# Performance work log

Hardware: AMD Instinct MI355X
Metric: run time of the kernel (lower is better)

The kernel has to match this reference:

```python
import jax, jax.numpy as jnp
import numpy as np
import math

B, S, D, H = 2, 2048, 1024, 16
HD = D // H  # head_dim = 64

def setup_inputs() -> dict:
    key = jax.random.key(0)
    ks = jax.random.split(key, 11)
    def n(k, shape, scale=1.0):
        return jax.random.normal(k, shape, dtype=jnp.float32) * scale
    w_scale = 1.0 / math.sqrt(D)
    return {
        "q": n(ks[0], (B, S, D)),
        "k": n(ks[1], (B, S, D)),
        "v": n(ks[2], (B, S, D)),
        "WQ_w": n(ks[3], (D, D), w_scale),
        "WQ_b": n(ks[4], (D,), 0.01),
        "WK_w": n(ks[5], (D, D), w_scale),
        "WK_b": n(ks[6], (D,), 0.01),
        "WV_w": n(ks[7], (D, D), w_scale),
        "WV_b": n(ks[8], (D,), 0.01),
        "Wout_w": n(ks[9], (D, D), w_scale),
        "Wout_b": n(ks[10], (D,), 0.01),
    }

def reference(q, k, v, WQ_w, WQ_b, WK_w, WK_b, WV_w, WV_b, Wout_w, Wout_b):
    b, s, _ = k.shape
    # QKV projections (torch Linear: x @ W.T + b; here weights stored [in, out])
    qh = (q @ WQ_w + WQ_b).reshape(b, -1, H, HD).transpose(0, 2, 1, 3)  # [b,h,s,hd]
    kh = (k @ WK_w + WK_b).reshape(b, -1, H, HD).transpose(0, 2, 1, 3)
    vh = (v @ WV_w + WV_b).reshape(b, -1, H, HD).transpose(0, 2, 1, 3)
    # naive attention: full [b,h,s,s] score matrix
    scores = jnp.einsum("bhqd,bhkd->bhqk", qh, kh) / math.sqrt(HD)
    attn = jax.nn.softmax(scores, axis=-1)
    out = jnp.einsum("bhqk,bhkd->bhqd", attn, vh)
    concat = out.transpose(0, 2, 1, 3).reshape(b, -1, H * HD)  # [b,s,inner_dim]
    return concat @ Wout_w + Wout_b
```

## Files before the change

kernel.cpp:

```cpp
#include <hip/hip_runtime.h>
#include <hip/hip_bf16.h>
#include <stdint.h>

typedef __attribute__((ext_vector_type(8))) short bf16x8;
typedef __attribute__((ext_vector_type(4))) short short4v;
typedef __attribute__((ext_vector_type(4))) float f32x4;

#define MFMA16x16x32 __builtin_amdgcn_mfma_f32_16x16x32_bf16
#define CL2F 0.18033688011112042f

__device__ __forceinline__ short f2b(float f) {
  union { float f; uint32_t u; } x;
  x.f = f;
  uint32_t u = x.u;
  uint32_t r = (u + 0x7FFFu + ((u >> 16) & 1u)) >> 16;
  return (short)(uint16_t)r;
}

__device__ __forceinline__ uint32_t cvt_pk_bf16(float lo, float hi) {
  uint32_t r;
  asm volatile("v_cvt_pk_bf16_f32 %0, %1, %2" : "=v"(r) : "v"(lo), "v"(hi));
  return r;
}
__device__ __forceinline__ float exp2_fast(float x) {
  float r;
  asm volatile("v_exp_f32 %0, %1" : "=v"(r) : "v"(x));
  return r;
}
__device__ __forceinline__ bf16x8 cvt8(const float4 a, const float4 b) {
  union { uint32_t u[4]; bf16x8 v; } o;
  o.u[0] = cvt_pk_bf16(a.x, a.y);
  o.u[1] = cvt_pk_bf16(a.z, a.w);
  o.u[2] = cvt_pk_bf16(b.x, b.y);
  o.u[3] = cvt_pk_bf16(b.z, b.w);
  return o.v;
}

__device__ __forceinline__ void async_copy16(const void* g, void* l) {
  __builtin_amdgcn_global_load_lds(
      (const __attribute__((address_space(1))) void*)g,
      (__attribute__((address_space(3))) void*)l, 16, 0, 0);
}

__global__ void prep_kernel(const float* __restrict__ W0,
                            const float* __restrict__ W1,
                            const float* __restrict__ W2,
                            const float* __restrict__ W3,
                            const float* __restrict__ q,
                            const float* __restrict__ k,
                            const float* __restrict__ v,
                            short* __restrict__ Wt,
                            short* __restrict__ xq,
                            short* __restrict__ xk,
                            short* __restrict__ xv) {
  __shared__ short tile[64][72];
  const int z = blockIdx.z;
  const int t = threadIdx.x;
  if (z < 4) {
    const float* W = (z == 0) ? W0 : (z == 1) ? W1 : (z == 2) ? W2 : W3;
    short* Wo = Wt + (size_t)z * 1024 * 1024;
    const int r0 = blockIdx.y * 64;
    const int c0 = blockIdx.x * 64;
#pragma unroll
    for (int i = 0; i < 4; ++i) {
      const int lin = i * 1024 + t * 4;
      const int r = lin >> 6, c = lin & 63;
      const float4 vv = *(const float4*)&W[(size_t)(r0 + r) * 1024 + c0 + c];
      tile[r][c + 0] = f2b(vv.x);
      tile[r][c + 1] = f2b(vv.y);
      tile[r][c + 2] = f2b(vv.z);
      tile[r][c + 3] = f2b(vv.w);
    }
    __syncthreads();
#pragma unroll
    for (int i = 0; i < 2; ++i) {
      const int lin = i * 2048 + t * 8;
      const int r = lin >> 6, c = lin & 63;
      bf16x8 ov;
#pragma unroll
      for (int jj = 0; jj < 8; ++jj) ov[jj] = tile[c + jj][r];
      *(bf16x8*)&Wo[(size_t)(c0 + r) * 1024 + r0 + c] = ov;
    }
  } else {
    const float* x = (z == 4) ? q : (z == 5) ? k : v;
    short* yp = (z == 4) ? xq : (z == 5) ? xk : xv;
    const int base = (blockIdx.y * 16 + blockIdx.x) * 256 + t;
#pragma unroll
    for (int j = 0; j < 8; ++j) {
      const int i = base + j * 65536;
      const float4 a = ((const float4*)x)[2 * i];
      const float4 b = ((const float4*)x)[2 * i + 1];
      ((bf16x8*)yp)[i] = cvt8(a, b);
    }
  }
}

__launch_bounds__(256, 2)
__global__ void gemm_qkv_kernel(const short* __restrict__ A0,
                                const short* __restrict__ A1,
                                const short* __restrict__ A2,
                                const short* __restrict__ WtBase,
                                const float* __restrict__ b0,
                                const float* __restrict__ b1,
                                const float* __restrict__ b2,
                                short* __restrict__ C0,
                                short* __restrict__ C1,
                                short* __restrict__ Vt,
                                int ybase) {
  const int K = 1024;
  __shared__ short As[128 * 64];
  __shared__ short Bs[128 * 64];

  const int y = blockIdx.y + ybase;
  const short* A = (y == 0) ? A0 : (y == 1) ? A1 : A2;
  const short* Wt = WtBase + (size_t)y * 1024 * 1024;
  const float* bias = (y == 0) ? b0 : (y == 1) ? b1 : b2;

  const int tm = blockIdx.x & 31;
  const int tn = blockIdx.x >> 5;
  const int m0 = tm * 128, n0 = tn * 128;

  const int tid = threadIdx.x;
  const int lane = tid & 63;
  const int w = tid >> 6;
  const int wr = w >> 1, wc = w & 1;
  const int hi = lane >> 4, cc = lane & 15;
  const int srow = lane >> 3, schunk = lane & 7;

  f32x4 acc[4][4] = {};

  for (int kt = 0; kt < 16; ++kt) {
    const int k0 = kt * 64;
#pragma unroll
    for (int i = 0; i < 4; ++i) {
      const int ri = w * 4 + i;
      const int row = ri * 8 + srow;
      const int gch = schunk ^ (row & 7);
      async_copy16(A + (size_t)(m0 + row) * K + (k0 + gch * 8), &As[ri * 512]);
      async_copy16(Wt + (size_t)(n0 + row) * K + (k0 + gch * 8), &Bs[ri * 512]);
    }
    __syncthreads();
#pragma unroll
    for (int kk = 0; kk < 2; ++kk) {
      bf16x8 af[4], bfr[4];
#pragma unroll
      for (int x = 0; x < 4; ++x) {
        const int gch = kk * 4 + hi;
        const int rowA = wr * 64 + x * 16 + cc;
        af[x] = *(const bf16x8*)&As[rowA * 64 + ((gch ^ (rowA & 7)) << 3)];
        const int rowB = wc * 64 + x * 16 + cc;
        bfr[x] = *(const bf16x8*)&Bs[rowB * 64 + ((gch ^ (rowB & 7)) << 3)];
      }
#pragma unroll
      for (int x = 0; x < 4; ++x)
#pragma unroll
        for (int yy = 0; yy < 4; ++yy)
          acc[x][yy] = MFMA16x16x32(af[x], bfr[yy], acc[x][yy], 0, 0, 0);
    }
    __syncthreads();
  }

  short* Cout = (y == 0) ? C0 : C1;
#pragma unroll
  for (int x = 0; x < 4; ++x) {
    const int rbase = m0 + wr * 64 + x * 16 + (hi << 2);
#pragma unroll
    for (int yy = 0; yy < 4; ++yy) {
      const int col = n0 + wc * 64 + yy * 16 + cc;
      const float bv = bias[col];
      if (y == 2) {
        const int b = rbase >> 11, s = rbase & 2047;
        const int hh = col >> 6, d = col & 63;
        short4v pack;
#pragma unroll
        for (int r = 0; r < 4; ++r) pack[r] = f2b(acc[x][yy][r] + bv);
        *(short4v*)&Vt[((size_t)(b * 16 + hh) * 64 + d) * 2048 + s] = pack;
      } else {
#pragma unroll
        for (int r = 0; r < 4; ++r) {
          float val = acc[x][yy][r] + bv;
          if (y == 0) val *= CL2F;
          Cout[(size_t)(rbase + r) * 1024 + col] = f2b(val);
        }
      }
    }
  }
}

__launch_bounds__(256, 2)
__global__ void gemm_out_kernel(const short* __restrict__ A,
                                const short* __restrict__ Wt,
                                const float* __restrict__ bias,
                                float* __restrict__ C) {
  const int N = 1024, K = 1024;
  __shared__ short As[128 * 64];
  __shared__ short Bs[128 * 64];

  const int tm = blockIdx.x & 31;
  const int tn = blockIdx.x >> 5;
  const int m0 = tm * 128, n0 = tn * 128;

  const int tid = threadIdx.x;
  const int lane = tid & 63;
  const int w = tid >> 6;
  const int wr = w >> 1, wc = w & 1;
  const int hi = lane >> 4, cc = lane & 15;
  const int srow = lane >> 3, schunk = lane & 7;

  f32x4 acc[4][4] = {};

  for (int kt = 0; kt < 16; ++kt) {
    const int k0 = kt * 64;
#pragma unroll
    for (int i = 0; i < 4; ++i) {
      const int ri = w * 4 + i;
      const int row = ri * 8 + srow;
      const int gch = schunk ^ (row & 7);
      async_copy16(A + (size_t)(m0 + row) * K + (k0 + gch * 8), &As[ri * 512]);
      async_copy16(Wt + (size_t)(n0 + row) * K + (k0 + gch * 8), &Bs[ri * 512]);
    }
    __syncthreads();
#pragma unroll
    for (int kk = 0; kk < 2; ++kk) {
      bf16x8 af[4], bfr[4];
#pragma unroll
      for (int x = 0; x < 4; ++x) {
        const int gch = kk * 4 + hi;
        const int rowA = wr * 64 + x * 16 + cc;
        af[x] = *(const bf16x8*)&As[rowA * 64 + ((gch ^ (rowA & 7)) << 3)];
        const int rowB = wc * 64 + x * 16 + cc;
        bfr[x] = *(const bf16x8*)&Bs[rowB * 64 + ((gch ^ (rowB & 7)) << 3)];
      }
#pragma unroll
      for (int x = 0; x < 4; ++x)
#pragma unroll
        for (int yy = 0; yy < 4; ++yy)
          acc[x][yy] = MFMA16x16x32(af[x], bfr[yy], acc[x][yy], 0, 0, 0);
    }
    __syncthreads();
  }

#pragma unroll
  for (int x = 0; x < 4; ++x) {
    const int rbase = m0 + wr * 64 + x * 16 + (hi << 2);
#pragma unroll
    for (int yy = 0; yy < 4; ++yy) {
      const int col = n0 + wc * 64 + yy * 16 + cc;
      const float bv = bias[col];
#pragma unroll
      for (int r = 0; r < 4; ++r)
        C[(size_t)(rbase + r) * N + col] = acc[x][yy][r] + bv;
    }
  }
}

__launch_bounds__(256, 2)
__global__ void attn_kernel(const short* __restrict__ qh,
                            const short* __restrict__ kh,
                            const short* __restrict__ Vt,
                            short* __restrict__ concat) {
  __shared__ short Ks[2][64 * 64];
  __shared__ short Vs[2][64 * 64];

  const int qb = blockIdx.x;
  const int h = blockIdx.y;
  const int b = blockIdx.z;
  const int tid = threadIdx.x, lane = tid & 63, w = tid >> 6;
  const int hi = lane >> 4, cc = lane & 15;

  const size_t rowbase = (size_t)b * 2048;
  const int q0 = qb * 128 + w * 32;

  bf16x8 qf[2][2];
#pragma unroll
  for (int aq = 0; aq < 2; ++aq)
#pragma unroll
    for (int kk = 0; kk < 2; ++kk) {
      const int col = h * 64 + kk * 32 + hi * 8;
      qf[aq][kk] =
          *(const bf16x8*)&qh[(rowbase + q0 + aq * 16 + cc) * 1024 + col];
    }

  f32x4 oacc[2][4] = {};
  float l[2] = {0.f, 0.f};
  bf16x8 vf[2][4];
  uint32_t pu[2][4][2];

  const short* Vth = Vt + (size_t)(b * 16 + h) * 64 * 2048;
  const int srow = lane >> 3, schunk = lane & 7;
  const int fKr = (((cc >> 2) & 1) << 2) | (cc & 3);

  auto STAGE = [&](int tile, int buf) {
#pragma unroll
    for (int i = 0; i < 2; ++i) {
      const int ri = w * 2 + i;
      const int row = ri * 8 + srow;
      const int gchK = schunk ^ ((((ri) & 1) << 2) | (srow & 3));
      const int gchV = schunk ^ (row & 7);
      async_copy16(&kh[(rowbase + tile * 64 + row) * 1024 + h * 64 + gchK * 8],
                   &Ks[buf][ri * 512]);
      async_copy16(&Vth[(size_t)row * 2048 + tile * 64 + gchV * 8],
                   &Vs[buf][ri * 512]);
    }
  };
  auto QK = [&](int buf, f32x4 (&sacc)[2][4]) {
#pragma unroll
    for (int kk = 0; kk < 2; ++kk) {
      bf16x8 kf[4];
#pragma unroll
      for (int n = 0; n < 4; ++n) {
        const int row = ((n >> 1) << 5) + (((cc >> 2)) << 3) + ((n & 1) << 2) +
                        (cc & 3);
        const int ch = (kk * 4 + hi) ^ fKr;
        kf[n] = *(const bf16x8*)&Ks[buf][row * 64 + (ch << 3)];
      }
#pragma unroll
      for (int aq = 0; aq < 2; ++aq)
#pragma unroll
        for (int n = 0; n < 4; ++n)
          sacc[aq][n] = MFMA16x16x32(kf[n], qf[aq][kk], sacc[aq][n], 0, 0, 0);
    }
  };
  auto LOADV = [&](int buf) {
#pragma unroll
    for (int kvh = 0; kvh < 2; ++kvh) {
      const int ch = (kvh * 4 + hi) ^ (cc & 7);
#pragma unroll
      for (int n = 0; n < 4; ++n)
        vf[kvh][n] =
            *(const bf16x8*)&Vs[buf][(n * 16 + cc) * 64 + (ch << 3)];
    }
  };
  auto SOFTMAX = [&](f32x4 (&sacc)[2][4]) {
#pragma unroll
    for (int aq = 0; aq < 2; ++aq)
#pragma unroll
      for (int n = 0; n < 4; ++n) {
        const float p0 = exp2_fast(sacc[aq][n][0]);
        const float p1 = exp2_fast(sacc[aq][n][1]);
        const float p2 = exp2_fast(sacc[aq][n][2]);
        const float p3 = exp2_fast(sacc[aq][n][3]);
        l[aq] += (p0 + p1) + (p2 + p3);
        pu[aq][n][0] = cvt_pk_bf16(p0, p1);
        pu[aq][n][1] = cvt_pk_bf16(p2, p3);
      }
  };
  auto PV = [&]() {
#pragma unroll
    for (int kvh = 0; kvh < 2; ++kvh)
#pragma unroll
      for (int aq = 0; aq < 2; ++aq) {
        union { uint32_t u[4]; bf16x8 v; } pf;
        pf.u[0] = pu[aq][2 * kvh][0];
        pf.u[1] = pu[aq][2 * kvh][1];
        pf.u[2] = pu[aq][2 * kvh + 1][0];
        pf.u[3] = pu[aq][2 * kvh + 1][1];
#pragma unroll
        for (int n = 0; n < 4; ++n)
          oacc[aq][n] = MFMA16x16x32(vf[kvh][n], pf.v, oacc[aq][n], 0, 0, 0);
      }
  };

  STAGE(0, 0);
  __syncthreads();
  {
    STAGE(1, 1);
    f32x4 sacc[2][4] = {};
    QK(0, sacc);
    LOADV(0);
    SOFTMAX(sacc);
    __syncthreads();
  }

  for (int t = 1; t < 32; ++t) {
    const int cur = t & 1;
    if (t + 1 < 32) STAGE(t + 1, cur ^ 1);
    f32x4 sacc[2][4] = {};
    QK(cur, sacc);
    PV();
    LOADV(cur);
    SOFTMAX(sacc);
    __syncthreads();
  }
  PV();

#pragma unroll
  for (int aq = 0; aq < 2; ++aq) {
    float lv = l[aq];
    lv += __shfl_xor(lv, 16);
    lv += __shfl_xor(lv, 32);
    const float inv = 1.0f / lv;
    const size_t grow = rowbase + q0 + aq * 16 + cc;
#pragma unroll
    for (int n = 0; n < 4; ++n)
#pragma unroll
      for (int r = 0; r < 4; ++r) {
        const int d = n * 16 + hi * 4 + r;
        concat[grow * 1024 + h * 64 + d] = f2b(oacc[aq][n][r] * inv);
      }
  }
}

extern "C" void kernel_launch(void* const* d_in, const int* in_sizes, int n_in,
                              void* d_out, int out_size, void* d_ws, size_t ws_size,
                              hipStream_t stream) {
  const float* q = (const float*)d_in[0];
  const float* k = (const float*)d_in[1];
  const float* v = (const float*)d_in[2];
  const float* WQ = (const float*)d_in[3];
  const float* bQ = (const float*)d_in[4];
  const float* WK = (const float*)d_in[5];
  const float* bK = (const float*)d_in[6];
  const float* WV = (const float*)d_in[7];
  const float* bV = (const float*)d_in[8];
  const float* WO = (const float*)d_in[9];
  const float* bO = (const float*)d_in[10];

  char* ws = (char*)d_ws;
  const size_t MB = 1024 * 1024;
  short* Wt = (short*)ws;
  short* xq = (short*)(ws + 8 * MB);
  short* xk = (short*)(ws + 16 * MB);
  short* xv = (short*)(ws + 24 * MB);
  short* qh = (short*)(ws + 32 * MB);
  short* kh = (short*)(ws + 40 * MB);
  short* concat = xk;

  prep_kernel<<<dim3(16, 16, 7), 256, 0, stream>>>(WQ, WK, WV, WO, q, k, v,
                                                   Wt, xq, xk, xv);

  if (ws_size >= 56 * MB) {
    short* Vt = (short*)(ws + 48 * MB);
    gemm_qkv_kernel<<<dim3(256, 3), 256, 0, stream>>>(
        xq, xk, xv, Wt, bQ, bK, bV, qh, kh, Vt, 0);
    attn_kernel<<<dim3(16, 16, 2), 256, 0, stream>>>(qh, kh, Vt, concat);
  } else {
    short* Vt = xq;
    gemm_qkv_kernel<<<dim3(256, 2), 256, 0, stream>>>(
        xq, xk, xv, Wt, bQ, bK, bV, qh, kh, Vt, 0);
    gemm_qkv_kernel<<<dim3(256, 1), 256, 0, stream>>>(
        xq, xk, xv, Wt, bQ, bK, bV, qh, kh, Vt, 2);
    attn_kernel<<<dim3(16, 16, 2), 256, 0, stream>>>(qh, kh, Vt, concat);
  }

  gemm_out_kernel<<<256, 256, 0, stream>>>(concat, Wt + 3 * MB, bO,
                                           (float*)d_out);
}
```

Before: 113.7 us.

## Load V fragments directly from global memory and reorder attention grid

V tiles are no longer staged through shared memory. Each wave reads its V fragments straight from global (L2) memory, which drops half the LDS traffic and footprint. The grid is remapped so that head and batch vary fastest across blocks, which should improve K/V reuse in cache across query blocks. MFMA sections are wrapped in s_setprio to favour matrix issue. The risk is that the direct global V loads, issued just before softmax, are not hidden by the pipeline and add latency.

```diff
diff --git a/kernel.cpp b/kernel.cpp
--- a/kernel.cpp
+++ b/kernel.cpp
@@ -260,11 +260,11 @@
                             const short* __restrict__ Vt,
                             short* __restrict__ concat) {
   __shared__ short Ks[2][64 * 64];
-  __shared__ short Vs[2][64 * 64];
-
-  const int qb = blockIdx.x;
-  const int h = blockIdx.y;
-  const int b = blockIdx.z;
+
+  const int hb = blockIdx.x;
+  const int qb = blockIdx.y;
+  const int h = hb & 15;
+  const int b = hb >> 4;
   const int tid = threadIdx.x, lane = tid & 63, w = tid >> 6;
   const int hi = lane >> 4, cc = lane & 15;
 
@@ -296,11 +296,8 @@
       const int ri = w * 2 + i;
       const int row = ri * 8 + srow;
       const int gchK = schunk ^ ((((ri) & 1) << 2) | (srow & 3));
-      const int gchV = schunk ^ (row & 7);
       async_copy16(&kh[(rowbase + tile * 64 + row) * 1024 + h * 64 + gchK * 8],
                    &Ks[buf][ri * 512]);
-      async_copy16(&Vth[(size_t)row * 2048 + tile * 64 + gchV * 8],
-                   &Vs[buf][ri * 512]);
     }
   };
   auto QK = [&](int buf, f32x4 (&sacc)[2][4]) {
@@ -314,22 +311,22 @@
         const int ch = (kk * 4 + hi) ^ fKr;
         kf[n] = *(const bf16x8*)&Ks[buf][row * 64 + (ch << 3)];
       }
+      __builtin_amdgcn_s_setprio(1);
 #pragma unroll
       for (int aq = 0; aq < 2; ++aq)
 #pragma unroll
         for (int n = 0; n < 4; ++n)
           sacc[aq][n] = MFMA16x16x32(kf[n], qf[aq][kk], sacc[aq][n], 0, 0, 0);
+      __builtin_amdgcn_s_setprio(0);
     }
   };
-  auto LOADV = [&](int buf) {
-#pragma unroll
-    for (int kvh = 0; kvh < 2; ++kvh) {
-      const int ch = (kvh * 4 + hi) ^ (cc & 7);
+  auto LOADV = [&](int tile) {
+#pragma unroll
+    for (int kvh = 0; kvh < 2; ++kvh)
 #pragma unroll
       for (int n = 0; n < 4; ++n)
-        vf[kvh][n] =
-            *(const bf16x8*)&Vs[buf][(n * 16 + cc) * 64 + (ch << 3)];
-    }
+        vf[kvh][n] = *(const bf16x8*)&Vth[(size_t)(n * 16 + cc) * 2048 +
+                                          tile * 64 + (kvh * 4 + hi) * 8];
   };
   auto SOFTMAX = [&](f32x4 (&sacc)[2][4]) {
 #pragma unroll
@@ -346,6 +343,7 @@
       }
   };
   auto PV = [&]() {
+    __builtin_amdgcn_s_setprio(1);
 #pragma unroll
     for (int kvh = 0; kvh < 2; ++kvh)
 #pragma unroll
@@ -359,6 +357,7 @@
         for (int n = 0; n < 4; ++n)
           oacc[aq][n] = MFMA16x16x32(vf[kvh][n], pf.v, oacc[aq][n], 0, 0, 0);
       }
+    __builtin_amdgcn_s_setprio(0);
   };
 
   STAGE(0, 0);
@@ -378,7 +377,7 @@
     f32x4 sacc[2][4] = {};
     QK(cur, sacc);
     PV();
-    LOADV(cur);
+    LOADV(t);
     SOFTMAX(sacc);
     __syncthreads();
   }
@@ -433,14 +432,14 @@
     short* Vt = (short*)(ws + 48 * MB);
     gemm_qkv_kernel<<<dim3(256, 3), 256, 0, stream>>>(
         xq, xk, xv, Wt, bQ, bK, bV, qh, kh, Vt, 0);
-    attn_kernel<<<dim3(16, 16, 2), 256, 0, stream>>>(qh, kh, Vt, concat);
+    attn_kernel<<<dim3(32, 16), 256, 0, stream>>>(qh, kh, Vt, concat);
   } else {
     short* Vt = xq;
     gemm_qkv_kernel<<<dim3(256, 2), 256, 0, stream>>>(
         xq, xk, xv, Wt, bQ, bK, bV, qh, kh, Vt, 0);
     gemm_qkv_kernel<<<dim3(256, 1), 256, 0, stream>>>(
         xq, xk, xv, Wt, bQ, bK, bV, qh, kh, Vt, 2);
-    attn_kernel<<<dim3(16, 16, 2), 256, 0, stream>>>(qh, kh, Vt, concat);
+    attn_kernel<<<dim3(32, 16), 256, 0, stream>>>(qh, kh, Vt, concat);
   }
 
   gemm_out_kernel<<<256, 256, 0, stream>>>(concat, Wt + 3 * MB, bO,
```

Measured after the change: 135.4 us. +19.1%, slower.
